# Performance work log

Hardware: AMD Instinct MI355X
Metric: run time of the kernel (lower is better)

Reference implementation:

```python
import jax, jax.numpy as jnp
import numpy as np

L, N, E, H = 2048, 4, 1024, 16
DH = E // H


def setup_inputs() -> dict:
    key = jax.random.key(0)
    k1, k2, k3 = jax.random.split(key, 3)
    x = jax.random.normal(k1, (L, N, E), dtype=jnp.float32)
    # init like nn.Linear-ish scale to keep activations sane
    weight_qkv = jax.random.normal(k2, (3 * E, E), dtype=jnp.float32) * (E ** -0.5)
    weight_out = jax.random.normal(k3, (E, E), dtype=jnp.float32) * (E ** -0.5)
    return {"x": x, "weight_qkv": weight_qkv, "weight_out": weight_out}


def reference(x, weight_qkv, weight_out):
    # x: [L, N, E]; weight_qkv: [3E, E]; weight_out: [E, E]
    l, n, e = x.shape
    # fused QKV projection (F.linear: x @ W^T)
    qkv = jnp.einsum('lne,fe->lnf', x, weight_qkv)          # [L, N, 3E]
    qkv = qkv.reshape(l, n, 3, H, DH)
    q, k, v = jnp.moveaxis(qkv, 2, 0)                       # each [L, N, H, DH]
    q = jnp.transpose(q, (1, 2, 0, 3))                      # [N, H, L, DH]
    k = jnp.transpose(k, (1, 2, 0, 3))
    v = jnp.transpose(v, (1, 2, 0, 3))
    scale = DH ** -0.5
    scores = jnp.einsum('nhld,nhmd->nhlm', q, k) * scale    # [N, H, L, L]
    attn = jax.nn.softmax(scores, axis=-1)                  # dropout p=0.0 -> identity
    ctx = jnp.einsum('nhlm,nhmd->nhld', attn, v)            # [N, H, L, DH]
    ctx = jnp.transpose(ctx, (2, 0, 1, 3)).reshape(l, n, e) # [L, N, E]
    out = jnp.einsum('lne,fe->lnf', ctx, weight_out)        # output projection
    return out
```

## Files before the change

### kernel.cpp

```cpp
#include <hip/hip_runtime.h>
#include <hip/hip_bf16.h>

#define SEQ_L 2048
#define NBATCH 4
#define EDIM 1024
#define NHEAD 16
#define DHEAD 64

typedef __attribute__((ext_vector_type(4))) float f32x4;
typedef __attribute__((ext_vector_type(8))) short short8;
typedef unsigned short u16;
typedef unsigned long long u64;

#define QSCALE (0.125f * 1.44269504088896340736f)

__device__ __forceinline__ u16 f2bf(float f){
  unsigned u = __float_as_uint(f);
  u += 0x7fffu + ((u >> 16) & 1u);
  return (u16)(u >> 16);
}
__device__ __forceinline__ unsigned cvt_pk_bf16(float a, float b){
  unsigned r;
  asm("v_cvt_pk_bf16_f32 %0, %1, %2" : "=v"(r) : "v"(a), "v"(b));
  return r;
}
__device__ __forceinline__ float fexp2(float x){
  float r; asm("v_exp_f32 %0, %1" : "=v"(r) : "v"(x)); return r;
}

__global__ __launch_bounds__(256) void cvt_f32_bf16(const float* __restrict__ src,
                                                    u16* __restrict__ dst, int n4){
  int i = blockIdx.x * 256 + threadIdx.x;
  if (i < n4){
    float4 v = reinterpret_cast<const float4*>(src)[i];
    uint2 o;
    o.x = cvt_pk_bf16(v.x, v.y);
    o.y = cvt_pk_bf16(v.z, v.w);
    *reinterpret_cast<uint2*>(dst + (size_t)i*4) = o;
  }
}

__global__ __launch_bounds__(256) void qkv_gemm(const u16* __restrict__ X,
                                                const u16* __restrict__ W,
                                                u16* __restrict__ Qd,
                                                u16* __restrict__ Kd,
                                                u16* __restrict__ Vt){
  __shared__ u16 SMEM[2*128*72];
  u16* XL = SMEM;
  u16* WL = SMEM + 128*72;
  const int tid = threadIdx.x;
  const int lane = tid & 63;
  const int wid = tid >> 6;
  const int wr = wid >> 1, wc = wid & 1;
  const int lr = lane & 15, lg = lane >> 4;
  const int bm = blockIdx.x, bn = blockIdx.y;
  f32x4 acc[4][4] = {};
  for (int kt = 0; kt < 16; ++kt){
    __syncthreads();
#pragma unroll
    for (int it = 0; it < 4; ++it){
      int c = tid + 256*it;
      int row = c >> 3, c8 = (c & 7) * 8;
      *(short8*)&XL[row*72 + c8] = *(const short8*)&X[(bm*128 + row)*EDIM + kt*64 + c8];
      *(short8*)&WL[row*72 + c8] = *(const short8*)&W[(bn*128 + row)*EDIM + kt*64 + c8];
    }
    __syncthreads();
#pragma unroll
    for (int ks = 0; ks < 2; ++ks){
      short8 a[4], b[4];
#pragma unroll
      for (int m = 0; m < 4; ++m)  a[m]  = *(short8*)&XL[(wr*64 + m*16  + lr)*72 + ks*32 + lg*8];
#pragma unroll
      for (int nn = 0; nn < 4; ++nn) b[nn] = *(short8*)&WL[(wc*64 + nn*16 + lr)*72 + ks*32 + lg*8];
#pragma unroll
      for (int m = 0; m < 4; ++m)
#pragma unroll
        for (int nn = 0; nn < 4; ++nn)
          acc[m][nn] = __builtin_amdgcn_mfma_f32_16x16x32_bf16(a[m], b[nn], acc[m][nn], 0, 0, 0);
    }
  }
  if (bn < 16){
#pragma unroll
    for (int m = 0; m < 4; ++m){
      const int i0 = bm*128 + wr*64 + m*16 + lg*4;
      const int l = i0 >> 2;
#pragma unroll
      for (int nn = 0; nn < 4; ++nn){
        const int f = bn*128 + wc*64 + nn*16 + lr;
        const int which = f >> 10;
        const int h = (f >> 6) & 15;
        const int d = f & 63;
        u16* dst = (which == 0) ? Qd : Kd;
        const float sc = (which == 0) ? QSCALE : 1.0f;
#pragma unroll
        for (int r = 0; r < 4; ++r)
          dst[((r*NHEAD + h)*SEQ_L + l)*DHEAD + d] = f2bf(acc[m][nn][r] * sc);
      }
    }
  } else {
    __syncthreads();
    u16* T = SMEM;
#pragma unroll
    for (int m = 0; m < 4; ++m){
      const int il0 = wr*64 + m*16 + lg*4;
#pragma unroll
      for (int nn = 0; nn < 4; ++nn){
        const int fl = wc*64 + nn*16 + lr;
        *(unsigned*)&T[fl*134 + il0]     = cvt_pk_bf16(acc[m][nn][0], acc[m][nn][1]);
        *(unsigned*)&T[fl*134 + il0 + 2] = cvt_pk_bf16(acc[m][nn][2], acc[m][nn][3]);
      }
    }
    __syncthreads();
    const int fl = tid & 127, nsel = tid >> 7;
    const int fV = bn*128 + fl - 2048;
    const int hh = fV >> 6, dd = fV & 63;
#pragma unroll
    for (int nn2 = 0; nn2 < 2; ++nn2){
      const int n = nsel*2 + nn2;
      u16 val[32];
#pragma unroll
      for (int ll = 0; ll < 32; ++ll)
        val[ll] = T[fl*134 + ll*4 + n];
      const size_t base = ((size_t)(n*NHEAD + hh)*DHEAD + dd)*SEQ_L + (size_t)bm*32;
#pragma unroll
      for (int j = 0; j < 4; ++j)
        *(short8*)&Vt[base + j*8] = *(short8*)&val[j*8];
    }
  }
}

__global__ __launch_bounds__(256) void attn(const u16* __restrict__ Qd,
                                            const u16* __restrict__ Kd,
                                            const u16* __restrict__ Vt,
                                            u16* __restrict__ Ctx){
  __shared__ u16 KL[128*72];
  __shared__ u16 VtL[64*136];
  __shared__ u16 PL[4*16*136];
  const int tid = threadIdx.x;
  const int lane = tid & 63;
  const int wid = tid >> 6;
  const int lr = lane & 15, lg = lane >> 4;
  const int head = blockIdx.y;
  const int n = head >> 4, h = head & 15;
  const u16* qh  = Qd + head * (SEQ_L * DHEAD);
  const u16* kh  = Kd + head * (SEQ_L * DHEAD);
  const u16* vth = Vt + (size_t)head * (DHEAD * SEQ_L);
  const int q0 = blockIdx.x * 64 + wid * 16;
  short8 bq[2];
#pragma unroll
  for (int ks = 0; ks < 2; ++ks)
    bq[ks] = *(const short8*)&qh[(q0 + lr)*DHEAD + ks*32 + lg*8];
  f32x4 acc[4] = {};
  float mrun = -1e30f, lrun = 0.0f;
  u16* myP = &PL[wid * 16 * 136];
  const int kr = tid >> 3, kc8 = (tid & 7) * 8;
  const int vr = tid >> 4, vc8 = (tid & 15) * 8;
  short8 kreg[4], vreg[4];
#pragma unroll
  for (int j = 0; j < 4; ++j){
    kreg[j] = *(const short8*)&kh[(j*32 + kr)*DHEAD + kc8];
    vreg[j] = *(const short8*)&vth[(size_t)(j*16 + vr)*SEQ_L + vc8];
  }

  for (int t = 0; t < SEQ_L/128; ++t){
    const int kb0 = t*128;
    __syncthreads();
#pragma unroll
    for (int j = 0; j < 4; ++j){
      *(short8*)&KL[(j*32 + kr)*72 + kc8]   = kreg[j];
      *(short8*)&VtL[(j*16 + vr)*136 + vc8] = vreg[j];
    }
    __syncthreads();
    if (t < SEQ_L/128 - 1){
      const int kn = kb0 + 128;
#pragma unroll
      for (int j = 0; j < 4; ++j){
        kreg[j] = *(const short8*)&kh[(kn + j*32 + kr)*DHEAD + kc8];
        vreg[j] = *(const short8*)&vth[(size_t)(j*16 + vr)*SEQ_L + kn + vc8];
      }
    }
    f32x4 s[8];
#pragma unroll
    for (int kb = 0; kb < 8; ++kb){
      short8 a0 = *(short8*)&KL[(kb*16 + lr)*72 + lg*8];
      short8 a1 = *(short8*)&KL[(kb*16 + lr)*72 + 32 + lg*8];
      f32x4 z = {0.f, 0.f, 0.f, 0.f};
      z = __builtin_amdgcn_mfma_f32_16x16x32_bf16(a0, bq[0], z, 0, 0, 0);
      z = __builtin_amdgcn_mfma_f32_16x16x32_bf16(a1, bq[1], z, 0, 0, 0);
      s[kb] = z;
    }
    float tmax = -1e30f;
#pragma unroll
    for (int kb = 0; kb < 8; ++kb)
      tmax = fmaxf(tmax, fmaxf(fmaxf(s[kb][0], s[kb][1]), fmaxf(s[kb][2], s[kb][3])));
    tmax = fmaxf(tmax, __shfl_xor(tmax, 16));
    tmax = fmaxf(tmax, __shfl_xor(tmax, 32));
    if (!__all(tmax <= mrun + 8.0f)){
      const float mnew = fmaxf(mrun, tmax);
      const float alpha = fexp2(mrun - mnew);
      lrun *= alpha;
      mrun = mnew;
      float ar[4];
#pragma unroll
      for (int r = 0; r < 4; ++r) ar[r] = __shfl(alpha, lg*4 + r);
#pragma unroll
      for (int db = 0; db < 4; ++db)
#pragma unroll
        for (int r = 0; r < 4; ++r) acc[db][r] *= ar[r];
    }
    float ps = 0.0f;
#pragma unroll
    for (int kb = 0; kb < 8; ++kb){
      const float p0 = fexp2(s[kb][0] - mrun);
      const float p1 = fexp2(s[kb][1] - mrun);
      const float p2 = fexp2(s[kb][2] - mrun);
      const float p3 = fexp2(s[kb][3] - mrun);
      const unsigned lo = cvt_pk_bf16(p0, p1);
      const unsigned hi = cvt_pk_bf16(p2, p3);
      *(u64*)&myP[lr*136 + kb*16 + lg*4] = ((u64)hi << 32) | (u64)lo;
      ps += (p0 + p1) + (p2 + p3);
    }
    ps += __shfl_xor(ps, 16);
    ps += __shfl_xor(ps, 32);
    lrun += ps;
    asm volatile("s_waitcnt lgkmcnt(0)" ::: "memory");
    __builtin_amdgcn_sched_barrier(0);
#pragma unroll
    for (int c = 0; c < 4; ++c){
      short8 ap = *(short8*)&myP[lr*136 + c*32 + lg*8];
#pragma unroll
      for (int db = 0; db < 4; ++db){
        short8 bv = *(short8*)&VtL[(db*16 + lr)*136 + c*32 + lg*8];
        acc[db] = __builtin_amdgcn_mfma_f32_16x16x32_bf16(ap, bv, acc[db], 0, 0, 0);
      }
    }
  }
#pragma unroll
  for (int r = 0; r < 4; ++r){
    const float ld = __shfl(lrun, lg*4 + r);
    const float inv = 1.0f / ld;
    const int ql = q0 + lg*4 + r;
#pragma unroll
    for (int db = 0; db < 4; ++db)
      Ctx[(ql*NBATCH + n)*EDIM + h*DHEAD + db*16 + lr] = f2bf(acc[db][r] * inv);
  }
}

__global__ __launch_bounds__(256) void out_gemm(const u16* __restrict__ X,
                                                const u16* __restrict__ W,
                                                float* __restrict__ O){
  __shared__ u16 XL[128*72];
  __shared__ u16 WL[128*72];
  const int tid = threadIdx.x;
  const int lane = tid & 63;
  const int wid = tid >> 6;
  const int wr = wid >> 1, wc = wid & 1;
  const int lr = lane & 15, lg = lane >> 4;
  const int bm = blockIdx.x, bn = blockIdx.y;
  f32x4 acc[4][4] = {};
  for (int kt = 0; kt < 16; ++kt){
    __syncthreads();
#pragma unroll
    for (int it = 0; it < 4; ++it){
      int c = tid + 256*it;
      int row = c >> 3, c8 = (c & 7) * 8;
      *(short8*)&XL[row*72 + c8] = *(const short8*)&X[(bm*128 + row)*EDIM + kt*64 + c8];
      *(short8*)&WL[row*72 + c8] = *(const short8*)&W[(bn*128 + row)*EDIM + kt*64 + c8];
    }
    __syncthreads();
#pragma unroll
    for (int ks = 0; ks < 2; ++ks){
      short8 a[4], b[4];
#pragma unroll
      for (int m = 0; m < 4; ++m)  a[m]  = *(short8*)&XL[(wr*64 + m*16  + lr)*72 + ks*32 + lg*8];
#pragma unroll
      for (int nn = 0; nn < 4; ++nn) b[nn] = *(short8*)&WL[(wc*64 + nn*16 + lr)*72 + ks*32 + lg*8];
#pragma unroll
      for (int m = 0; m < 4; ++m)
#pragma unroll
        for (int nn = 0; nn < 4; ++nn)
          acc[m][nn] = __builtin_amdgcn_mfma_f32_16x16x32_bf16(a[m], b[nn], acc[m][nn], 0, 0, 0);
    }
  }
#pragma unroll
  for (int m = 0; m < 4; ++m){
    const int i0 = bm*128 + wr*64 + m*16 + lg*4;
#pragma unroll
    for (int nn = 0; nn < 4; ++nn){
      const int f = bn*128 + wc*64 + nn*16 + lr;
#pragma unroll
      for (int r = 0; r < 4; ++r)
        O[(size_t)(i0 + r)*EDIM + f] = acc[m][nn][r];
    }
  }
}

extern "C" void kernel_launch(void* const* d_in, const int* in_sizes, int n_in,
                              void* d_out, int out_size, void* d_ws, size_t ws_size,
                              hipStream_t stream){
  const float* x    = (const float*)d_in[0];
  const float* wqkv = (const float*)d_in[1];
  const float* wout = (const float*)d_in[2];
  float* out = (float*)d_out;
  u16* ws = (u16*)d_ws;
  const size_t XN  = (size_t)SEQ_L * NBATCH * EDIM;
  const size_t WQN = (size_t)3 * EDIM * EDIM;
  const size_t WON = (size_t)EDIM * EDIM;
  u16* xb    = ws;
  u16* wqkvb = xb + XN;
  u16* woutb = wqkvb + WQN;
  u16* qd    = woutb + WON;
  u16* kd    = qd + XN;
  u16* vt    = kd + XN;
  u16* ctx   = xb;

  cvt_f32_bf16<<<(int)(XN  / 1024), 256, 0, stream>>>(x,    xb,    (int)(XN  / 4));
  cvt_f32_bf16<<<(int)(WQN / 1024), 256, 0, stream>>>(wqkv, wqkvb, (int)(WQN / 4));
  cvt_f32_bf16<<<(int)(WON / 1024), 256, 0, stream>>>(wout, woutb, (int)(WON / 4));
  qkv_gemm<<<dim3(64, 24), 256, 0, stream>>>(xb, wqkvb, qd, kd, vt);
  attn    <<<dim3(32, 64), 256, 0, stream>>>(qd, kd, vt, ctx);
  out_gemm<<<dim3(64, 8),  256, 0, stream>>>(ctx, woutb, out);
}
```

Before: 245.0 us.

## Rewrite attention with 32x32x16 MFMA keeping P in registers

The attention kernel now uses 32x32x16 bf16 MFMAs. Each wave handles 32 queries, each block handles 128 queries, and K/V tiles are 64 wide. The score output layout is arranged (via a permuted K row store) so the exponentiated probabilities feed directly as the A operand of the PV MFMA. This removes the P round trip through LDS and its waitcnt. It also halves the grid, which lowers parallelism and adds register pressure from the 16-wide accumulators.

After: 229.6 us. 6.3% less time.

```diff
diff --git a/kernel.cpp b/kernel.cpp
--- a/kernel.cpp
+++ b/kernel.cpp
@@ -8,6 +8,7 @@
 #define DHEAD 64
 
 typedef __attribute__((ext_vector_type(4))) float f32x4;
+typedef __attribute__((ext_vector_type(16))) float f32x16;
 typedef __attribute__((ext_vector_type(8))) short short8;
 typedef unsigned short u16;
 typedef unsigned long long u64;
@@ -133,116 +134,104 @@
                                             const u16* __restrict__ Kd,
                                             const u16* __restrict__ Vt,
                                             u16* __restrict__ Ctx){
-  __shared__ u16 KL[128*72];
-  __shared__ u16 VtL[64*136];
-  __shared__ u16 PL[4*16*136];
+  __shared__ u16 KL[64*66];
+  __shared__ u16 VtL[64*66];
   const int tid = threadIdx.x;
   const int lane = tid & 63;
   const int wid = tid >> 6;
-  const int lr = lane & 15, lg = lane >> 4;
+  const int l31 = lane & 31, hf = lane >> 5;
   const int head = blockIdx.y;
   const int n = head >> 4, h = head & 15;
   const u16* qh  = Qd + head * (SEQ_L * DHEAD);
   const u16* kh  = Kd + head * (SEQ_L * DHEAD);
   const u16* vth = Vt + (size_t)head * (DHEAD * SEQ_L);
-  const int q0 = blockIdx.x * 64 + wid * 16;
-  short8 bq[2];
-#pragma unroll
-  for (int ks = 0; ks < 2; ++ks)
-    bq[ks] = *(const short8*)&qh[(q0 + lr)*DHEAD + ks*32 + lg*8];
-  f32x4 acc[4] = {};
+  const int q0 = blockIdx.x * 128 + wid * 32;
+  short8 bq[4];
+#pragma unroll
+  for (int st = 0; st < 4; ++st)
+    bq[st] = *(const short8*)&qh[(q0 + l31)*DHEAD + st*16 + hf*8];
+  f32x16 acc[2] = {};
   float mrun = -1e30f, lrun = 0.0f;
-  u16* myP = &PL[wid * 16 * 136];
-  const int kr = tid >> 3, kc8 = (tid & 7) * 8;
-  const int vr = tid >> 4, vc8 = (tid & 15) * 8;
-  short8 kreg[4], vreg[4];
-#pragma unroll
-  for (int j = 0; j < 4; ++j){
-    kreg[j] = *(const short8*)&kh[(j*32 + kr)*DHEAD + kc8];
-    vreg[j] = *(const short8*)&vth[(size_t)(j*16 + vr)*SEQ_L + vc8];
-  }
-
-  for (int t = 0; t < SEQ_L/128; ++t){
-    const int kb0 = t*128;
-    __syncthreads();
-#pragma unroll
-    for (int j = 0; j < 4; ++j){
-      *(short8*)&KL[(j*32 + kr)*72 + kc8]   = kreg[j];
-      *(short8*)&VtL[(j*16 + vr)*136 + vc8] = vreg[j];
-    }
-    __syncthreads();
-    if (t < SEQ_L/128 - 1){
-      const int kn = kb0 + 128;
-#pragma unroll
-      for (int j = 0; j < 4; ++j){
-        kreg[j] = *(const short8*)&kh[(kn + j*32 + kr)*DHEAD + kc8];
-        vreg[j] = *(const short8*)&vth[(size_t)(j*16 + vr)*SEQ_L + kn + vc8];
-      }
-    }
-    f32x4 s[8];
-#pragma unroll
-    for (int kb = 0; kb < 8; ++kb){
-      short8 a0 = *(short8*)&KL[(kb*16 + lr)*72 + lg*8];
-      short8 a1 = *(short8*)&KL[(kb*16 + lr)*72 + 32 + lg*8];
-      f32x4 z = {0.f, 0.f, 0.f, 0.f};
-      z = __builtin_amdgcn_mfma_f32_16x16x32_bf16(a0, bq[0], z, 0, 0, 0);
-      z = __builtin_amdgcn_mfma_f32_16x16x32_bf16(a1, bq[1], z, 0, 0, 0);
-      s[kb] = z;
-    }
-    float tmax = -1e30f;
-#pragma unroll
-    for (int kb = 0; kb < 8; ++kb)
-      tmax = fmaxf(tmax, fmaxf(fmaxf(s[kb][0], s[kb][1]), fmaxf(s[kb][2], s[kb][3])));
-    tmax = fmaxf(tmax, __shfl_xor(tmax, 16));
-    tmax = fmaxf(tmax, __shfl_xor(tmax, 32));
-    if (!__all(tmax <= mrun + 8.0f)){
-      const float mnew = fmaxf(mrun, tmax);
-      const float alpha = fexp2(mrun - mnew);
-      lrun *= alpha;
-      mrun = mnew;
-      float ar[4];
-#pragma unroll
-      for (int r = 0; r < 4; ++r) ar[r] = __shfl(alpha, lg*4 + r);
-#pragma unroll
-      for (int db = 0; db < 4; ++db)
-#pragma unroll
-        for (int r = 0; r < 4; ++r) acc[db][r] *= ar[r];
-    }
-    float ps = 0.0f;
-#pragma unroll
-    for (int kb = 0; kb < 8; ++kb){
-      const float p0 = fexp2(s[kb][0] - mrun);
-      const float p1 = fexp2(s[kb][1] - mrun);
-      const float p2 = fexp2(s[kb][2] - mrun);
-      const float p3 = fexp2(s[kb][3] - mrun);
-      const unsigned lo = cvt_pk_bf16(p0, p1);
-      const unsigned hi = cvt_pk_bf16(p2, p3);
-      *(u64*)&myP[lr*136 + kb*16 + lg*4] = ((u64)hi << 32) | (u64)lo;
-      ps += (p0 + p1) + (p2 + p3);
-    }
-    ps += __shfl_xor(ps, 16);
-    ps += __shfl_xor(ps, 32);
-    lrun += ps;
-    asm volatile("s_waitcnt lgkmcnt(0)" ::: "memory");
-    __builtin_amdgcn_sched_barrier(0);
-#pragma unroll
-    for (int c = 0; c < 4; ++c){
-      short8 ap = *(short8*)&myP[lr*136 + c*32 + lg*8];
-#pragma unroll
-      for (int db = 0; db < 4; ++db){
-        short8 bv = *(short8*)&VtL[(db*16 + lr)*136 + c*32 + lg*8];
-        acc[db] = __builtin_amdgcn_mfma_f32_16x16x32_bf16(ap, bv, acc[db], 0, 0, 0);
-      }
-    }
-  }
-#pragma unroll
-  for (int r = 0; r < 4; ++r){
-    const float ld = __shfl(lrun, lg*4 + r);
-    const float inv = 1.0f / ld;
-    const int ql = q0 + lg*4 + r;
-#pragma unroll
-    for (int db = 0; db < 4; ++db)
-      Ctx[(ql*NBATCH + n)*EDIM + h*DHEAD + db*16 + lr] = f2bf(acc[db][r] * inv);
+  const int srow = tid >> 3, sc8 = (tid & 7) * 8;
+  const int prow = (srow & ~12) | ((srow & 4) << 1) | ((srow & 8) >> 1);
+  short8 kreg[2], vreg[2];
+#pragma unroll
+  for (int j = 0; j < 2; ++j){
+    kreg[j] = *(const short8*)&kh[(j*32 + srow)*DHEAD + sc8];
+    vreg[j] = *(const short8*)&vth[(size_t)(j*32 + srow)*SEQ_L + sc8];
+  }
+
+  for (int t = 0; t < SEQ_L/64; ++t){
+    __syncthreads();
+    *(short8*)&KL[prow*66 + sc8]       = kreg[0];
+    *(short8*)&KL[(prow+32)*66 + sc8]  = kreg[1];
+    *(short8*)&VtL[srow*66 + sc8]      = vreg[0];
+    *(short8*)&VtL[(srow+32)*66 + sc8] = vreg[1];
+    __syncthreads();
+    if (t < SEQ_L/64 - 1){
+      const int kn = (t + 1) * 64;
+#pragma unroll
+      for (int j = 0; j < 2; ++j){
+        kreg[j] = *(const short8*)&kh[(kn + j*32 + srow)*DHEAD + sc8];
+        vreg[j] = *(const short8*)&vth[(size_t)(j*32 + srow)*SEQ_L + kn + sc8];
+      }
+    }
+#pragma unroll
+    for (int c = 0; c < 2; ++c){
+      f32x16 sD = {0.f,0.f,0.f,0.f,0.f,0.f,0.f,0.f,0.f,0.f,0.f,0.f,0.f,0.f,0.f,0.f};
+#pragma unroll
+      for (int st = 0; st < 4; ++st){
+        short8 ak = *(short8*)&KL[(c*32 + l31)*66 + st*16 + hf*8];
+        sD = __builtin_amdgcn_mfma_f32_32x32x16_bf16(ak, bq[st], sD, 0, 0, 0);
+      }
+      float tmax = sD[0];
+#pragma unroll
+      for (int r = 1; r < 16; ++r) tmax = fmaxf(tmax, sD[r]);
+      tmax = fmaxf(tmax, __shfl_xor(tmax, 32));
+      if (!__all(tmax <= mrun + 8.0f)){
+        const float mnew = fmaxf(mrun, tmax);
+        const float alpha = fexp2(mrun - mnew);
+        lrun *= alpha;
+        mrun = mnew;
+#pragma unroll
+        for (int r = 0; r < 16; ++r){
+          const float aq = __shfl(alpha, (r&3) + 8*(r>>2) + 4*hf);
+          acc[0][r] *= aq;
+          acc[1][r] *= aq;
+        }
+      }
+      float p[16];
+      float ps = 0.f;
+#pragma unroll
+      for (int r = 0; r < 16; ++r){
+        p[r] = fexp2(sD[r] - mrun);
+        ps += p[r];
+      }
+      ps += __shfl_xor(ps, 32);
+      lrun += ps;
+#pragma unroll
+      for (int s = 0; s < 2; ++s){
+        union { unsigned u[4]; short8 s8; } pa;
+#pragma unroll
+        for (int jj = 0; jj < 4; ++jj)
+          pa.u[jj] = cvt_pk_bf16(p[s*8 + jj*2], p[s*8 + jj*2 + 1]);
+#pragma unroll
+        for (int db = 0; db < 2; ++db){
+          short8 bv = *(short8*)&VtL[(db*32 + l31)*66 + c*32 + s*16 + hf*8];
+          acc[db] = __builtin_amdgcn_mfma_f32_32x32x16_bf16(pa.s8, bv, acc[db], 0, 0, 0);
+        }
+      }
+    }
+  }
+#pragma unroll
+  for (int r = 0; r < 16; ++r){
+    const int ql = (r&3) + 8*(r>>2) + 4*hf;
+    const float denom = __shfl(lrun, ql);
+    const float inv = 1.0f / denom;
+    const int q = q0 + ql;
+#pragma unroll
+    for (int db = 0; db < 2; ++db)
+      Ctx[(q*NBATCH + n)*EDIM + h*DHEAD + db*32 + l31] = f2bf(acc[db][r] * inv);
   }
 }
 
@@ -318,6 +307,6 @@
   cvt_f32_bf16<<<(int)(WQN / 1024), 256, 0, stream>>>(wqkv, wqkvb, (int)(WQN / 4));
   cvt_f32_bf16<<<(int)(WON / 1024), 256, 0, stream>>>(wout, woutb, (int)(WON / 4));
   qkv_gemm<<<dim3(64, 24), 256, 0, stream>>>(xb, wqkvb, qd, kd, vt);
-  attn    <<<dim3(32, 64), 256, 0, stream>>>(qd, kd, vt, ctx);
+  attn    <<<dim3(16, 64), 256, 0, stream>>>(qd, kd, vt, ctx);
   out_gemm<<<dim3(64, 8),  256, 0, stream>>>(ctx, woutb, out);
 }
```
